# Kernel tuning notes

Hardware: AMD Instinct MI355X
Metric: run time of the kernel (lower is better)

Reference implementation:

```python
import jax, jax.numpy as jnp
import numpy as np

NEG_SLOPE = 0.2
EPS = 1e-16


def setup_inputs() -> dict:
    key = jax.random.key(0)
    k1, k2, k3, k4, k5 = jax.random.split(key, 5)
    N, E, F_IN, H, C = 100000, 1600000, 128, 4, 32
    x = jax.random.normal(k1, (N, F_IN), dtype=jnp.float32)
    edge_index = jax.random.randint(k2, (2, E), 0, N, dtype=jnp.int64)
    W = jax.random.normal(k3, (F_IN, H * C), dtype=jnp.float32) * (1.0 / np.sqrt(F_IN))
    att_src = jax.random.normal(k4, (H, C), dtype=jnp.float32) * 0.1
    att_dst = jax.random.normal(k5, (H, C), dtype=jnp.float32) * 0.1
    bias = jnp.zeros((H * C,), dtype=jnp.float32)
    return {"x": x, "edge_index": edge_index, "W": W, "att_src": att_src,
            "att_dst": att_dst, "bias": bias}


def reference(x, edge_index, W, att_src, att_dst, bias):
    N = x.shape[0]
    H, C = att_src.shape
    # PyG GATConv default: add self-loops
    loops = jnp.arange(N, dtype=edge_index.dtype)
    src = jnp.concatenate([edge_index[0], loops])  # [E+N]
    dst = jnp.concatenate([edge_index[1], loops])  # [E+N]

    h = (x @ W).reshape(N, H, C)                  # [N,H,C]
    a_src = jnp.einsum('nhc,hc->nh', h, att_src)  # [N,H]
    a_dst = jnp.einsum('nhc,hc->nh', h, att_dst)  # [N,H]

    e = a_src[src] + a_dst[dst]                   # [E',H]
    e = jax.nn.leaky_relu(e, NEG_SLOPE)

    # segment softmax over destination nodes (numerically stable)
    m = jax.ops.segment_max(e, dst, num_segments=N)      # [N,H]
    p = jnp.exp(e - m[dst])                               # [E',H]
    s = jax.ops.segment_sum(p, dst, num_segments=N)       # [N,H]
    alpha = p / (s[dst] + EPS)                             # [E',H]

    msg = h[src] * alpha[:, :, None]                       # [E',H,C]
    out = jax.ops.segment_sum(msg, dst, num_segments=N)   # [N,H,C]
    return out.reshape(N, H * C) + bias
```

## Files before the change

kernel.cpp:

```cpp
#include <hip/hip_runtime.h>
#include <stdint.h>


#define SLOT 64
#define CNTS 16
#define BCNS 16
#define BCAP 1536
#define MAXB 2048
#define KCH  8192

typedef __attribute__((ext_vector_type(8))) _Float16 h8;
typedef __attribute__((ext_vector_type(4))) float    f4x;

__device__ __forceinline__ float b2f(unsigned short u) {
    union { unsigned int i; float f; } v; v.i = ((unsigned int)u) << 16; return v.f;
}
__device__ __forceinline__ unsigned short f2b(float f) {
    union { float f; unsigned int i; } v; v.f = f;
    unsigned int i = v.i;
    unsigned int r = (i + 0x7FFFu + ((i >> 16) & 1u)) >> 16;
    return (unsigned short)r;
}
__device__ __forceinline__ unsigned short f2h(float f) {
    union { _Float16 h; unsigned short u; } v; v.h = (_Float16)f; return v.u;
}
__device__ __forceinline__ float h2f(unsigned short u) {
    union { _Float16 h; unsigned short u; } v; v.u = u; return (float)v.h;
}

__global__ void k_detect(const int* __restrict__ eidx, const unsigned int* __restrict__ xw,
                         int* flags) {
    __shared__ int nz, bf;
    if (threadIdx.x == 0) { nz = 0; bf = 0; }
    __syncthreads();
    int bad = 0;
    for (int i = threadIdx.x; i < 1024; i += 256)
        if (eidx[2 * i + 1] != 0) bad = 1;
    if (bad) atomicOr(&nz, 1);
    int hits = 0;
    for (int i = threadIdx.x; i < 4096; i += 256) {
        unsigned int e = (xw[i] >> 7) & 0xFFu;
        if (e >= 0x60u && e < 0xA0u) ++hits;
    }
    atomicAdd(&bf, hits);
    __syncthreads();
    if (threadIdx.x == 0) {
        flags[0] = (nz == 0) ? 1 : 0;
        flags[1] = (bf > 3072) ? 1 : 0;
    }
}

__device__ __forceinline__ int edge_at(const int* idx32, const long long* idx64,
                                       int is64, long long pos) {
    return is64 ? (int)idx64[pos] : idx32[pos];
}

__global__ void k_prep(const void* __restrict__ Wv, const void* __restrict__ asv,
                       const void* __restrict__ adv, const void* __restrict__ bv,
                       const int* __restrict__ flags,
                       _Float16* __restrict__ Wth, _Float16* __restrict__ Wtl,
                       float* __restrict__ attf , float* __restrict__ biasf ) {
    int isbf = flags[1];
    int tid = blockIdx.x * 256 + threadIdx.x;
    for (int i = tid; i < 16384; i += gridDim.x * 256) {
        int col = i >> 7, k = i & 127;
        float w = isbf ? b2f(((const unsigned short*)Wv)[k * 128 + col])
                       : ((const float*)Wv)[k * 128 + col];
        unsigned short hi = f2h(w);
        unsigned short lo = f2h(w - h2f(hi));
        ((unsigned short*)Wth)[i] = hi;
        ((unsigned short*)Wtl)[i] = lo;
    }
    if (blockIdx.x == 0) {
        for (int i = threadIdx.x; i < 128; i += 256) {
            attf[i]       = isbf ? b2f(((const unsigned short*)asv)[i]) : ((const float*)asv)[i];
            attf[128 + i] = isbf ? b2f(((const unsigned short*)adv)[i]) : ((const float*)adv)[i];
            biasf[i]      = isbf ? b2f(((const unsigned short*)bv)[i]) : ((const float*)bv)[i];
        }
    }
}

__global__ __launch_bounds__(256) void k_gemm_scatter(
    const void* __restrict__ xv,
    const _Float16* __restrict__ Wth, const _Float16* __restrict__ Wtl,
    const float* __restrict__ attf, const int* __restrict__ flags,
    unsigned short* __restrict__ hbf, float* __restrict__ asf,
    float* __restrict__ adf, int N,
    const int* __restrict__ idx32, const long long* __restrict__ idx64,
    int* __restrict__ bcnt, unsigned* __restrict__ bdat,
    int* __restrict__ cnt, int* __restrict__ esrc,
    int E, int Gg, int SB) {
    __shared__ unsigned short xsh[64 * 128];
    __shared__ unsigned short xsl[64 * 128];
    int tid = threadIdx.x;
    int bid = blockIdx.x;

    if (bid < SB) {
        int is64 = flags[0];
        int NBK = (N + 63) >> 6;
        long long e0 = (long long)bid * KCH;
        long long e1 = e0 + KCH; if (e1 > E) e1 = E;
        if (e0 >= E) return;

        if (NBK <= MAXB) {
            int wid = tid >> 6;
            int* h0 = (int*)xsh; int* h1 = h0 + MAXB;
            int* h2 = (int*)xsl; int* h3 = h2 + MAXB;
            int* hw = (wid == 0) ? h0 : (wid == 1) ? h1 : (wid == 2) ? h2 : h3;
            for (int i = tid; i < NBK; i += 256) { h0[i] = 0; h1[i] = 0; h2[i] = 0; h3[i] = 0; }
            __syncthreads();
            for (long long e = e0 + tid; e < e1; e += 256) {
                int d = is64 ? (int)idx64[(long long)E + e] : idx32[E + e];
                atomicAdd(&hw[d >> 6], 1);
            }
            __syncthreads();
            for (int b = tid; b < NBK; b += 256) {
                int c0 = h0[b], c1 = h1[b], c2 = h2[b], c3 = h3[b];
                int t = c0 + c1 + c2 + c3;
                int base = (t > 0) ? atomicAdd(&bcnt[(size_t)b * BCNS], t) : 0;
                h0[b] = base;
                h1[b] = base + c0;
                h2[b] = base + c0 + c1;
                h3[b] = base + c0 + c1 + c2;
            }
            __syncthreads();
            for (long long e = e0 + tid; e < e1; e += 256) {
                int d, s;
                if (is64) {
                    d = (int)idx64[(long long)E + e]; s = (int)idx64[e];
                } else {
                    d = idx32[E + e]; s = idx32[e];
                }
                int b = d >> 6;
                int p = atomicAdd(&hw[b], 1);
                if (p < BCAP)
                    bdat[(size_t)b * BCAP + p] = (unsigned)s | ((unsigned)(d & 63) << 26);
            }
        } else {
            for (long long e = e0 + tid; e < e1; e += 256) {
                int d = edge_at(idx32, idx64, is64, (long long)E + e);
                int s = edge_at(idx32, idx64, is64, e);
                int p = atomicAdd(&cnt[(size_t)d * CNTS], 1);
                if (p < SLOT) esrc[(size_t)d * SLOT + p] = s;
            }
        }
        return;
    }

    int rb = bid - SB;
    if (rb >= Gg) return;
    int r0 = rb * 64;
    int isbf = flags[1];
    int w = tid >> 6;
    int lane = tid & 63;
    int li = lane & 15;
    int g  = lane >> 4;
    int c0 = w * 32;

    h8 Bh[2][4], Bl[2][4];
#pragma unroll
    for (int t = 0; t < 2; ++t)
#pragma unroll
        for (int s = 0; s < 4; ++s) {
            size_t o = (size_t)(c0 + 16 * t + li) * 128 + 32 * s + 8 * g;
            Bh[t][s] = *(const h8*)(Wth + o);
            Bl[t][s] = *(const h8*)(Wtl + o);
        }

#pragma unroll
    for (int it = 0; it < 4; ++it) {
        int idx = it * 2048 + tid * 8;
        int r = idx >> 7, k = idx & 127;
        int gr = r0 + r; if (gr >= N) gr = N - 1;
        float v[8];
        if (isbf) {
            uint4 raw = *(const uint4*)((const unsigned short*)xv + (size_t)gr * 128 + k);
            v[0] = b2f((unsigned short)(raw.x & 0xFFFFu)); v[1] = b2f((unsigned short)(raw.x >> 16));
            v[2] = b2f((unsigned short)(raw.y & 0xFFFFu)); v[3] = b2f((unsigned short)(raw.y >> 16));
            v[4] = b2f((unsigned short)(raw.z & 0xFFFFu)); v[5] = b2f((unsigned short)(raw.z >> 16));
            v[6] = b2f((unsigned short)(raw.w & 0xFFFFu)); v[7] = b2f((unsigned short)(raw.w >> 16));
        } else {
            const float* xf = (const float*)xv;
            float4 a = *(const float4*)(xf + (size_t)gr * 128 + k);
            float4 b = *(const float4*)(xf + (size_t)gr * 128 + k + 4);
            v[0] = a.x; v[1] = a.y; v[2] = a.z; v[3] = a.w;
            v[4] = b.x; v[5] = b.y; v[6] = b.z; v[7] = b.w;
        }
        uint4 PH, PL;
        unsigned int ph[4], pl[4];
#pragma unroll
        for (int jj = 0; jj < 4; ++jj) {
            unsigned short h0 = f2h(v[2 * jj]), h1 = f2h(v[2 * jj + 1]);
            unsigned short l0 = f2h(v[2 * jj] - h2f(h0));
            unsigned short l1 = f2h(v[2 * jj + 1] - h2f(h1));
            ph[jj] = (unsigned int)h0 | ((unsigned int)h1 << 16);
            pl[jj] = (unsigned int)l0 | ((unsigned int)l1 << 16);
        }
        PH.x = ph[0]; PH.y = ph[1]; PH.z = ph[2]; PH.w = ph[3];
        PL.x = pl[0]; PL.y = pl[1]; PL.z = pl[2]; PL.w = pl[3];
        int off = r * 256 + ((2 * k) ^ ((r & 7) << 4));
        *(uint4*)((char*)xsh + off) = PH;
        *(uint4*)((char*)xsl + off) = PL;
    }
    __syncthreads();

    f4x acc[4][2];
#pragma unroll
    for (int m = 0; m < 4; ++m)
#pragma unroll
        for (int t = 0; t < 2; ++t) acc[m][t] = (f4x){0.f, 0.f, 0.f, 0.f};

#pragma unroll
    for (int s = 0; s < 4; ++s) {
#pragma unroll
        for (int m = 0; m < 4; ++m) {
            int row = 16 * m + li;
            int kb = (32 * s + 8 * g) * 2;
            int off = row * 256 + (kb ^ ((row & 7) << 4));
            h8 ah = *(const h8*)((const char*)xsh + off);
            h8 al = *(const h8*)((const char*)xsl + off);
#pragma unroll
            for (int t = 0; t < 2; ++t) {
                acc[m][t] = __builtin_amdgcn_mfma_f32_16x16x32_f16(ah, Bh[t][s], acc[m][t], 0, 0, 0);
                acc[m][t] = __builtin_amdgcn_mfma_f32_16x16x32_f16(al, Bh[t][s], acc[m][t], 0, 0, 0);
                acc[m][t] = __builtin_amdgcn_mfma_f32_16x16x32_f16(ah, Bl[t][s], acc[m][t], 0, 0, 0);
            }
        }
    }

    float at_s0 = attf[c0 + li],       at_s1 = attf[c0 + 16 + li];
    float at_d0 = attf[128 + c0 + li], at_d1 = attf[128 + c0 + 16 + li];
#pragma unroll
    for (int m = 0; m < 4; ++m) {
        float s1v[4], s2v[4];
#pragma unroll
        for (int j = 0; j < 4; ++j) {
            s1v[j] = acc[m][0][j] * at_s0 + acc[m][1][j] * at_s1;
            s2v[j] = acc[m][0][j] * at_d0 + acc[m][1][j] * at_d1;
        }
#pragma unroll
        for (int j = 0; j < 4; ++j) {
#pragma unroll
            for (int msk = 1; msk < 16; msk <<= 1) {
                s1v[j] += __shfl_xor(s1v[j], msk);
                s2v[j] += __shfl_xor(s2v[j], msk);
            }
        }
        if (li == 0) {
#pragma unroll
            for (int j = 0; j < 4; ++j) {
                int gr = r0 + 16 * m + 4 * g + j;
                if (gr < N) {
                    asf[(size_t)gr * 4 + w] = s1v[j];
                    adf[(size_t)gr * 4 + w] = s2v[j];
                }
            }
        }
    }

    __syncthreads();
#pragma unroll
    for (int m = 0; m < 4; ++m)
#pragma unroll
        for (int t = 0; t < 2; ++t)
#pragma unroll
            for (int j = 0; j < 4; ++j)
                xsh[(16 * m + 4 * g + j) * 128 + c0 + 16 * t + li] = f2b(acc[m][t][j]);
    __syncthreads();
#pragma unroll
    for (int it = 0; it < 4; ++it) {
        int u = it * 2048 + tid * 8;
        int r = u >> 7, k = u & 127;
        int gr = r0 + r;
        if (gr < N)
            *(uint4*)(hbf + (size_t)gr * 128 + k) = *(const uint4*)(xsh + u);
    }
}

template <int NB>
__device__ __forceinline__ void agg_node(
    int n, int dl, int deg, int lane, int head,
    const int lslot[64][SLOT], float* psh,
    const unsigned short* __restrict__ hbf,
    const float* __restrict__ asf, const float* __restrict__ adf,
    float& a0o, float& a1o, float& invho) {
    int sl = (lane == 0) ? n : ((lane <= deg) ? lslot[dl][lane - 1] : n);
    float4 av, adv;
    asm volatile("global_load_dwordx4 %0, %1, off"
                 : "=v"(av) : "v"((const void*)(asf + (size_t)sl * 4)));
    asm volatile("global_load_dwordx4 %0, %1, off"
                 : "=v"(adv) : "v"((const void*)(adf + (size_t)n * 4)));
    unsigned vv[NB * 8];
#pragma unroll
    for (int it = 0; it < NB * 8; ++it) {
        int s = (it == 0) ? n : ((it <= deg) ? lslot[dl][it - 1] : n);
        asm volatile("global_load_dword %0, %1, off"
                     : "=v"(vv[it]) : "v"((const void*)(hbf + (size_t)s * 128 + 2 * lane)));
    }
    asm volatile("s_waitcnt vmcnt(%0)" :: "n"(NB * 8));
    __builtin_amdgcn_sched_barrier(0);

    float p0 = 0.f, p1 = 0.f, p2 = 0.f, p3 = 0.f;
    if (lane <= deg) {
        float e0 = av.x + adv.x; e0 = fmaxf(e0, 0.2f * e0); p0 = __expf(e0);
        float e1 = av.y + adv.y; e1 = fmaxf(e1, 0.2f * e1); p1 = __expf(e1);
        float e2 = av.z + adv.z; e2 = fmaxf(e2, 0.2f * e2); p2 = __expf(e2);
        float e3 = av.w + adv.w; e3 = fmaxf(e3, 0.2f * e3); p3 = __expf(e3);
    }
    psh[0 * 64 + lane] = p0; psh[1 * 64 + lane] = p1;
    psh[2 * 64 + lane] = p2; psh[3 * 64 + lane] = p3;
    __builtin_amdgcn_wave_barrier();
    asm volatile("s_waitcnt lgkmcnt(0)" ::: "memory");
    __builtin_amdgcn_wave_barrier();

    float ps0 = p0, ps1 = p1, ps2 = p2, ps3 = p3;
#pragma unroll
    for (int m = 1; m < 64; m <<= 1) {
        ps0 += __shfl_xor(ps0, m);
        ps1 += __shfl_xor(ps1, m);
        ps2 += __shfl_xor(ps2, m);
        ps3 += __shfl_xor(ps3, m);
    }
    float den = head == 0 ? ps0 : head == 1 ? ps1 : head == 2 ? ps2 : ps3;
    invho = 1.0f / (den + 1e-16f);

    float a0 = 0.f, a1 = 0.f;
#pragma unroll
    for (int bi = 0; bi < NB; ++bi) {
        asm volatile("s_waitcnt vmcnt(%0)" :: "n"(8 * (NB - 1 - bi)));
        __builtin_amdgcn_sched_barrier(0);
        float4 qa = *(const float4*)(psh + head * 64 + bi * 8);
        float4 qb = *(const float4*)(psh + head * 64 + bi * 8 + 4);
#pragma unroll
        for (int k2 = 0; k2 < 8; ++k2) {
            float q = k2 < 4 ? qa[k2] : qb[k2 - 4];
            unsigned v = vv[bi * 8 + k2];
            a0 += q * b2f((unsigned short)v);
            a1 += q * b2f((unsigned short)(v >> 16));
        }
    }
    a0o = a0; a1o = a1;
}

__global__ __launch_bounds__(256) void k_bagg(
    const unsigned* __restrict__ bdat, const int* __restrict__ bcnt,
    const unsigned short* __restrict__ hbf,
    const float* __restrict__ asf, const float* __restrict__ adf,
    const int* __restrict__ idx32, const long long* __restrict__ idx64,
    const float* __restrict__ biasf, const int* __restrict__ flags,
    void* __restrict__ outv, int N, int E) {
    __shared__ int   lcnt[64];
    __shared__ int   lslot[64][SLOT];
    __shared__ float p_all[4][SLOT * 4];
    int b = blockIdx.x, tid = threadIdx.x;
    int wid = tid >> 6, lane = tid & 63, head = lane >> 4;

    if (tid < 64) lcnt[tid] = 0;
    __syncthreads();
    int mm = bcnt[(size_t)b * BCNS];
    int ovf = (mm > BCAP);
    if (mm > BCAP) mm = BCAP;
    for (int i = tid; i < mm; i += 256) {
        unsigned e = bdat[(size_t)b * BCAP + i];
        int dl = (int)(e >> 26);
        int p = atomicAdd(&lcnt[dl], 1);
        if (p < SLOT) lslot[dl][p] = (int)(e & 0x03FFFFFFu);
    }
    __syncthreads();

    float b0 = biasf[2 * lane], b1 = biasf[2 * lane + 1];
    float* psh = p_all[wid];
    int isbf = flags[1];
    int is64 = flags[0];

    for (int u = 0; u < 16; ++u) {
        int dl = wid * 16 + u;
        int n = (b << 6) + dl;
        if (n >= N) break;
        int deg = lcnt[dl];
        bool fb = ovf || (deg > SLOT - 1);
        float a0 = 0.f, a1 = 0.f, invh = 0.f;

        if (!fb && deg <= 31) {
            int nb = (deg + 8) >> 3;
            switch (nb) {
                case 1: agg_node<1>(n, dl, deg, lane, head, lslot, psh, hbf, asf, adf, a0, a1, invh); break;
                case 2: agg_node<2>(n, dl, deg, lane, head, lslot, psh, hbf, asf, adf, a0, a1, invh); break;
                case 3: agg_node<3>(n, dl, deg, lane, head, lslot, psh, hbf, asf, adf, a0, a1, invh); break;
                default: agg_node<4>(n, dl, deg, lane, head, lslot, psh, hbf, asf, adf, a0, a1, invh); break;
            }
        } else if (!fb) {
            float4 adv = *(const float4*)(adf + (size_t)n * 4);
            int sl = (lane == 0) ? n : ((lane <= deg) ? lslot[dl][lane - 1] : n);
            float4 av = *(const float4*)(asf + (size_t)sl * 4);
            float p0 = 0.f, p1 = 0.f, p2 = 0.f, p3 = 0.f;
            if (lane <= deg) {
                float e0 = av.x + adv.x; e0 = fmaxf(e0, 0.2f * e0); p0 = __expf(e0);
                float e1 = av.y + adv.y; e1 = fmaxf(e1, 0.2f * e1); p1 = __expf(e1);
                float e2 = av.z + adv.z; e2 = fmaxf(e2, 0.2f * e2); p2 = __expf(e2);
                float e3 = av.w + adv.w; e3 = fmaxf(e3, 0.2f * e3); p3 = __expf(e3);
            }
            psh[0 * 64 + lane] = p0; psh[1 * 64 + lane] = p1;
            psh[2 * 64 + lane] = p2; psh[3 * 64 + lane] = p3;
            __builtin_amdgcn_wave_barrier();
            asm volatile("s_waitcnt lgkmcnt(0)" ::: "memory");
            __builtin_amdgcn_wave_barrier();
            float ps0 = p0, ps1 = p1, ps2 = p2, ps3 = p3;
#pragma unroll
            for (int m = 1; m < 64; m <<= 1) {
                ps0 += __shfl_xor(ps0, m);
                ps1 += __shfl_xor(ps1, m);
                ps2 += __shfl_xor(ps2, m);
                ps3 += __shfl_xor(ps3, m);
            }
            float den = head == 0 ? ps0 : head == 1 ? ps1 : head == 2 ? ps2 : ps3;
            invh = 1.0f / (den + 1e-16f);
            int nb = (deg + 8) >> 3;
            for (int bi = 0; bi < nb; ++bi) {
                unsigned vt[8];
#pragma unroll
                for (int k2 = 0; k2 < 8; ++k2) {
                    int it = bi * 8 + k2;
                    int s = (it == 0) ? n : ((it <= deg) ? lslot[dl][it - 1] : n);
                    vt[k2] = *(const unsigned int*)(hbf + (size_t)s * 128 + 2 * lane);
                }
                float4 qa = *(const float4*)(psh + head * 64 + bi * 8);
                float4 qb = *(const float4*)(psh + head * 64 + bi * 8 + 4);
#pragma unroll
                for (int k2 = 0; k2 < 8; ++k2) {
                    float q = k2 < 4 ? qa[k2] : qb[k2 - 4];
                    a0 += q * b2f((unsigned short)vt[k2]);
                    a1 += q * b2f((unsigned short)(vt[k2] >> 16));
                }
            }
        } else {
            float4 adv = *(const float4*)(adf + (size_t)n * 4);
            float adh = head == 0 ? adv.x : head == 1 ? adv.y : head == 2 ? adv.z : adv.w;
            float den = 0.f;
            {
                float ev = asf[(size_t)n * 4 + head] + adh; ev = fmaxf(ev, 0.2f * ev);
                float p = __expf(ev);
                unsigned int v = *(const unsigned int*)(hbf + (size_t)n * 128 + 2 * lane);
                den += p;
                a0 += p * b2f((unsigned short)v);
                a1 += p * b2f((unsigned short)(v >> 16));
            }
            for (int e = 0; e < E; ++e) {
                int d = edge_at(idx32, idx64, is64, (long long)E + e);
                if (d == n) {
                    int s = edge_at(idx32, idx64, is64, e);
                    float ev = asf[(size_t)s * 4 + head] + adh; ev = fmaxf(ev, 0.2f * ev);
                    float p = __expf(ev);
                    unsigned int v = *(const unsigned int*)(hbf + (size_t)s * 128 + 2 * lane);
                    den += p;
                    a0 += p * b2f((unsigned short)v);
                    a1 += p * b2f((unsigned short)(v >> 16));
                }
            }
            invh = 1.0f / (den + 1e-16f);
        }

        a0 = a0 * invh + b0;
        a1 = a1 * invh + b1;
        if (isbf) {
            unsigned int pk = (unsigned int)f2b(a0) | ((unsigned int)f2b(a1) << 16);
            ((unsigned int*)outv)[(size_t)n * 64 + lane] = pk;
        } else {
            float2 f2; f2.x = a0; f2.y = a1;
            *(float2*)((float*)outv + (size_t)n * 128 + 2 * lane) = f2;
        }
        __builtin_amdgcn_wave_barrier();
    }
}

__global__ __launch_bounds__(256) void k_aggregate(
    const unsigned short* __restrict__ hbf,
    const float* __restrict__ asf, const float* __restrict__ adf,
    const int* __restrict__ cnt, const int* __restrict__ esrc,
    const int* __restrict__ idx32, const long long* __restrict__ idx64,
    const float* __restrict__ biasf, const int* __restrict__ flags,
    void* __restrict__ outv, int N, int E) {
    __shared__ float p_sh_all[4][SLOT * 4];
    __shared__ int   s_sh_all[4][SLOT];
    int wid = threadIdx.x >> 6;
    int lane = threadIdx.x & 63;
    int n = blockIdx.x * 4 + wid;
    if (n >= N) n = N - 1;
    float* p_sh = p_sh_all[wid];
    int*   s_sh = s_sh_all[wid];
    int head = lane >> 4;

    int deg = cnt[(size_t)n * CNTS];
    float4 adv = *(const float4*)(adf + (size_t)n * 4);
    bool fb = (deg > SLOT - 1);

    float p0 = 0.f, p1 = 0.f, p2 = 0.f, p3 = 0.f;
    if (!fb && lane <= deg) {
        int s = (lane == 0) ? n : esrc[(size_t)n * SLOT + lane - 1];
        float4 av = *(const float4*)(asf + (size_t)s * 4);
        float e0 = av.x + adv.x; e0 = fmaxf(e0, 0.2f * e0); p0 = __expf(e0);
        float e1 = av.y + adv.y; e1 = fmaxf(e1, 0.2f * e1); p1 = __expf(e1);
        float e2 = av.z + adv.z; e2 = fmaxf(e2, 0.2f * e2); p2 = __expf(e2);
        float e3 = av.w + adv.w; e3 = fmaxf(e3, 0.2f * e3); p3 = __expf(e3);
        s_sh[lane] = s;
        p_sh[lane * 4 + 0] = p0; p_sh[lane * 4 + 1] = p1;
        p_sh[lane * 4 + 2] = p2; p_sh[lane * 4 + 3] = p3;
    }
    __syncthreads();

    float b0 = biasf[2 * lane], b1 = biasf[2 * lane + 1];
    float a0 = 0.f, a1 = 0.f, invh;

    if (!fb) {
        float ps0 = p0, ps1 = p1, ps2 = p2, ps3 = p3;
#pragma unroll
        for (int m = 1; m < 64; m <<= 1) {
            ps0 += __shfl_xor(ps0, m);
            ps1 += __shfl_xor(ps1, m);
            ps2 += __shfl_xor(ps2, m);
            ps3 += __shfl_xor(ps3, m);
        }
        float den = head == 0 ? ps0 : head == 1 ? ps1 : head == 2 ? ps2 : ps3;
        invh = 1.0f / (den + 1e-16f);

        int tot = deg + 1;
        int i = 0;
        for (; i + 3 < tot; i += 4) {
            int s0 = s_sh[i], s1 = s_sh[i + 1], s2 = s_sh[i + 2], s3 = s_sh[i + 3];
            float q0 = p_sh[i * 4 + head],       q1 = p_sh[(i + 1) * 4 + head];
            float q2 = p_sh[(i + 2) * 4 + head], q3 = p_sh[(i + 3) * 4 + head];
            unsigned int v0 = *(const unsigned int*)(hbf + (size_t)s0 * 128 + 2 * lane);
            unsigned int v1 = *(const unsigned int*)(hbf + (size_t)s1 * 128 + 2 * lane);
            unsigned int v2 = *(const unsigned int*)(hbf + (size_t)s2 * 128 + 2 * lane);
            unsigned int v3 = *(const unsigned int*)(hbf + (size_t)s3 * 128 + 2 * lane);
            a0 += q0 * b2f((unsigned short)v0) + q1 * b2f((unsigned short)v1)
                + q2 * b2f((unsigned short)v2) + q3 * b2f((unsigned short)v3);
            a1 += q0 * b2f((unsigned short)(v0 >> 16)) + q1 * b2f((unsigned short)(v1 >> 16))
                + q2 * b2f((unsigned short)(v2 >> 16)) + q3 * b2f((unsigned short)(v3 >> 16));
        }
        for (; i < tot; ++i) {
            int s0 = s_sh[i];
            float q0 = p_sh[i * 4 + head];
            unsigned int v0 = *(const unsigned int*)(hbf + (size_t)s0 * 128 + 2 * lane);
            a0 += q0 * b2f((unsigned short)v0);
            a1 += q0 * b2f((unsigned short)(v0 >> 16));
        }
    } else {
        int is64 = flags[0];
        float adh = head == 0 ? adv.x : head == 1 ? adv.y : head == 2 ? adv.z : adv.w;
        float den = 0.f;
        {
            float ev = asf[(size_t)n * 4 + head] + adh; ev = fmaxf(ev, 0.2f * ev);
            float p = __expf(ev);
            unsigned int v = *(const unsigned int*)(hbf + (size_t)n * 128 + 2 * lane);
            den += p;
            a0 += p * b2f((unsigned short)v);
            a1 += p * b2f((unsigned short)(v >> 16));
        }
        for (int e = 0; e < E; ++e) {
            int d = edge_at(idx32, idx64, is64, (long long)E + e);
            if (d == n) {
                int s = edge_at(idx32, idx64, is64, e);
                float ev = asf[(size_t)s * 4 + head] + adh; ev = fmaxf(ev, 0.2f * ev);
                float p = __expf(ev);
                unsigned int v = *(const unsigned int*)(hbf + (size_t)s * 128 + 2 * lane);
                den += p;
                a0 += p * b2f((unsigned short)v);
                a1 += p * b2f((unsigned short)(v >> 16));
            }
        }
        invh = 1.0f / (den + 1e-16f);
    }

    a0 = a0 * invh + b0;
    a1 = a1 * invh + b1;
    if (flags[1]) {
        unsigned int pk = (unsigned int)f2b(a0) | ((unsigned int)f2b(a1) << 16);
        ((unsigned int*)outv)[(size_t)n * 64 + lane] = pk;
    } else {
        float2 f2; f2.x = a0; f2.y = a1;
        *(float2*)((float*)outv + (size_t)n * 128 + 2 * lane) = f2;
    }
}

extern "C" void kernel_launch(void* const* d_in, const int* in_sizes, int n_in,
                              void* d_out, int out_size, void* d_ws, size_t ws_size,
                              hipStream_t stream) {
    const void*      xv    = d_in[0];
    const int*       idx32 = (const int*)d_in[1];
    const long long* idx64 = (const long long*)d_in[1];

    int N = in_sizes[0] / 128;
    int E = in_sizes[1] / 2;

    char* ws = (char*)d_ws;
    size_t o = 0;
    auto alloc = [&](size_t bytes) {
        size_t r = o; o += (bytes + 255) & ~(size_t)255; return r;
    };
    unsigned short* hbf = (unsigned short*)(ws + alloc((size_t)N * 128 * 2));
    _Float16* Wth = (_Float16*)(ws + alloc(16384 * 2));
    _Float16* Wtl = (_Float16*)(ws + alloc(16384 * 2));
    float* attf  = (float*)(ws + alloc(256 * 4));
    float* biasf = (float*)(ws + alloc(128 * 4));
    float* asf   = (float*)(ws + alloc((size_t)N * 4 * 4));
    float* adf   = (float*)(ws + alloc((size_t)N * 4 * 4));
    int* cnt     = (int*)(ws + alloc((size_t)N * CNTS * 4));
    int* flags   = (int*)(ws + alloc(256));
    int* esrc    = (int*)(ws + alloc((size_t)N * SLOT * 4));
    int NBK = (N + 63) >> 6;
    int* bcnt      = (int*)(ws + alloc((size_t)NBK * BCNS * 4));
    unsigned* bdat = (unsigned*)(ws + alloc((size_t)NBK * BCAP * 4));

    int Gg = (N + 63) / 64;
    int SB = (E + KCH - 1) / KCH;
    int NB = SB + Gg;

    k_detect<<<1, 256, 0, stream>>>(idx32, (const unsigned int*)xv, flags);
    k_prep<<<16, 256, 0, stream>>>(d_in[2], d_in[3], d_in[4], d_in[5], flags, Wth, Wtl, attf, biasf);
    if (NBK <= MAXB) {
        hipMemsetAsync(bcnt, 0, (size_t)NBK * BCNS * 4, stream);
        k_gemm_scatter<<<NB, 256, 0, stream>>>(xv, Wth, Wtl, attf, flags, hbf, asf, adf, N,
                                               idx32, idx64, bcnt, bdat, cnt, esrc, E, Gg, SB);
        k_bagg<<<NBK, 256, 0, stream>>>(bdat, bcnt, hbf, asf, adf, idx32, idx64,
                                        biasf, flags, d_out, N, E);
    } else {
        hipMemsetAsync(cnt, 0, (size_t)N * CNTS * 4, stream);
        k_gemm_scatter<<<NB, 256, 0, stream>>>(xv, Wth, Wtl, attf, flags, hbf, asf, adf, N,
                                               idx32, idx64, bcnt, bdat, cnt, esrc, E, Gg, SB);
        k_aggregate<<<(N + 3) / 4, 256, 0, stream>>>(hbf, asf, adf, cnt, esrc, idx32, idx64,
                                                     biasf, flags, d_out, N, E);
    }
}
```

Before: 273.6 us.

## Split wave into two half-waves gathering alternate neighbors with dwordx2 loads

The common low-degree aggregation path now splits each 64-lane wave into two 32-lane halves. Each half handles alternate neighbor rows, and each lane loads 4 bf16 features with a dwordx2 load instead of 2 with a single dword. The halves are then combined with a cross-lane shuffle and only the lower half writes the output. This halves the number of serial gather load instructions per node and the template depth (NB 1-2 instead of 1-4). In exchange it adds a reduction shuffle, per-element LDS reads of attention weights, and a padded LDS stride (68).

Measured after the change: 254.0 us. -7.2%, faster.

```diff
diff --git a/kernel.cpp b/kernel.cpp
--- a/kernel.cpp
+++ b/kernel.cpp
@@ -8,9 +8,11 @@
 #define BCAP 1536
 #define MAXB 2048
 #define KCH  8192
+#define PST  68
 
 typedef __attribute__((ext_vector_type(8))) _Float16 h8;
 typedef __attribute__((ext_vector_type(4))) float    f4x;
+typedef __attribute__((ext_vector_type(2))) unsigned u32x2;
 
 __device__ __forceinline__ float b2f(unsigned short u) {
     union { unsigned int i; float f; } v; v.i = ((unsigned int)u) << 16; return v.f;
@@ -278,24 +280,28 @@
 }
 
 template <int NB>
-__device__ __forceinline__ void agg_node(
-    int n, int dl, int deg, int lane, int head,
+__device__ __forceinline__ void agg_node2(
+    int n, int dl, int deg, int lane,
     const int lslot[64][SLOT], float* psh,
     const unsigned short* __restrict__ hbf,
     const float* __restrict__ asf, const float* __restrict__ adf,
-    float& a0o, float& a1o, float& invho) {
+    float a[4], float& invho) {
+    int half = lane >> 5;
+    int cl = lane & 31;
+    int hd = cl >> 3;
     int sl = (lane == 0) ? n : ((lane <= deg) ? lslot[dl][lane - 1] : n);
     float4 av, adv;
     asm volatile("global_load_dwordx4 %0, %1, off"
                  : "=v"(av) : "v"((const void*)(asf + (size_t)sl * 4)));
     asm volatile("global_load_dwordx4 %0, %1, off"
                  : "=v"(adv) : "v"((const void*)(adf + (size_t)n * 4)));
-    unsigned vv[NB * 8];
-#pragma unroll
-    for (int it = 0; it < NB * 8; ++it) {
+    u32x2 vv[NB * 8];
+#pragma unroll
+    for (int k = 0; k < NB * 8; ++k) {
+        int it = 2 * k + half;
         int s = (it == 0) ? n : ((it <= deg) ? lslot[dl][it - 1] : n);
-        asm volatile("global_load_dword %0, %1, off"
-                     : "=v"(vv[it]) : "v"((const void*)(hbf + (size_t)s * 128 + 2 * lane)));
+        asm volatile("global_load_dwordx2 %0, %1, off"
+                     : "=v"(vv[k]) : "v"((const void*)(hbf + (size_t)s * 128 + 4 * cl)));
     }
     asm volatile("s_waitcnt vmcnt(%0)" :: "n"(NB * 8));
     __builtin_amdgcn_sched_barrier(0);
@@ -307,8 +313,8 @@
         float e2 = av.z + adv.z; e2 = fmaxf(e2, 0.2f * e2); p2 = __expf(e2);
         float e3 = av.w + adv.w; e3 = fmaxf(e3, 0.2f * e3); p3 = __expf(e3);
     }
-    psh[0 * 64 + lane] = p0; psh[1 * 64 + lane] = p1;
-    psh[2 * 64 + lane] = p2; psh[3 * 64 + lane] = p3;
+    psh[0 * PST + lane] = p0; psh[1 * PST + lane] = p1;
+    psh[2 * PST + lane] = p2; psh[3 * PST + lane] = p3;
     __builtin_amdgcn_wave_barrier();
     asm volatile("s_waitcnt lgkmcnt(0)" ::: "memory");
     __builtin_amdgcn_wave_barrier();
@@ -321,25 +327,24 @@
         ps2 += __shfl_xor(ps2, m);
         ps3 += __shfl_xor(ps3, m);
     }
-    float den = head == 0 ? ps0 : head == 1 ? ps1 : head == 2 ? ps2 : ps3;
+    float den = hd == 0 ? ps0 : hd == 1 ? ps1 : hd == 2 ? ps2 : ps3;
     invho = 1.0f / (den + 1e-16f);
 
-    float a0 = 0.f, a1 = 0.f;
 #pragma unroll
     for (int bi = 0; bi < NB; ++bi) {
         asm volatile("s_waitcnt vmcnt(%0)" :: "n"(8 * (NB - 1 - bi)));
         __builtin_amdgcn_sched_barrier(0);
-        float4 qa = *(const float4*)(psh + head * 64 + bi * 8);
-        float4 qb = *(const float4*)(psh + head * 64 + bi * 8 + 4);
 #pragma unroll
         for (int k2 = 0; k2 < 8; ++k2) {
-            float q = k2 < 4 ? qa[k2] : qb[k2 - 4];
-            unsigned v = vv[bi * 8 + k2];
-            a0 += q * b2f((unsigned short)v);
-            a1 += q * b2f((unsigned short)(v >> 16));
-        }
-    }
-    a0o = a0; a1o = a1;
+            int it = 2 * (bi * 8 + k2) + half;
+            float q = psh[hd * PST + it];
+            u32x2 v = vv[bi * 8 + k2];
+            a[0] += q * b2f((unsigned short)v[0]);
+            a[1] += q * b2f((unsigned short)(v[0] >> 16));
+            a[2] += q * b2f((unsigned short)v[1]);
+            a[3] += q * b2f((unsigned short)(v[1] >> 16));
+        }
+    }
 }
 
 __global__ __launch_bounds__(256) void k_bagg(
@@ -351,7 +356,7 @@
     void* __restrict__ outv, int N, int E) {
     __shared__ int   lcnt[64];
     __shared__ int   lslot[64][SLOT];
-    __shared__ float p_all[4][SLOT * 4];
+    __shared__ float p_all[4][4 * PST];
     int b = blockIdx.x, tid = threadIdx.x;
     int wid = tid >> 6, lane = tid & 63, head = lane >> 4;
 
@@ -368,7 +373,9 @@
     }
     __syncthreads();
 
+    int cl = lane & 31;
     float b0 = biasf[2 * lane], b1 = biasf[2 * lane + 1];
+    float4 bq4 = *(const float4*)(biasf + 4 * cl);
     float* psh = p_all[wid];
     int isbf = flags[1];
     int is64 = flags[0];
@@ -379,17 +386,30 @@
         if (n >= N) break;
         int deg = lcnt[dl];
         bool fb = ovf || (deg > SLOT - 1);
-        float a0 = 0.f, a1 = 0.f, invh = 0.f;
 
         if (!fb && deg <= 31) {
-            int nb = (deg + 8) >> 3;
-            switch (nb) {
-                case 1: agg_node<1>(n, dl, deg, lane, head, lslot, psh, hbf, asf, adf, a0, a1, invh); break;
-                case 2: agg_node<2>(n, dl, deg, lane, head, lslot, psh, hbf, asf, adf, a0, a1, invh); break;
-                case 3: agg_node<3>(n, dl, deg, lane, head, lslot, psh, hbf, asf, adf, a0, a1, invh); break;
-                default: agg_node<4>(n, dl, deg, lane, head, lslot, psh, hbf, asf, adf, a0, a1, invh); break;
+            float a4[4] = {0.f, 0.f, 0.f, 0.f};
+            float invh = 0.f;
+            int nb = (deg + 16) >> 4;
+            if (nb == 1) agg_node2<1>(n, dl, deg, lane, lslot, psh, hbf, asf, adf, a4, invh);
+            else         agg_node2<2>(n, dl, deg, lane, lslot, psh, hbf, asf, adf, a4, invh);
+#pragma unroll
+            for (int c = 0; c < 4; ++c) a4[c] += __shfl_xor(a4[c], 32);
+            float o0 = a4[0] * invh + bq4.x, o1 = a4[1] * invh + bq4.y;
+            float o2 = a4[2] * invh + bq4.z, o3 = a4[3] * invh + bq4.w;
+            if (lane < 32) {
+                if (isbf) {
+                    u32x2 pk;
+                    pk[0] = (unsigned)f2b(o0) | ((unsigned)f2b(o1) << 16);
+                    pk[1] = (unsigned)f2b(o2) | ((unsigned)f2b(o3) << 16);
+                    *(u32x2*)((unsigned*)outv + (size_t)n * 64 + cl * 2) = pk;
+                } else {
+                    float4 f4v; f4v.x = o0; f4v.y = o1; f4v.z = o2; f4v.w = o3;
+                    *(float4*)((float*)outv + (size_t)n * 128 + cl * 4) = f4v;
+                }
             }
         } else if (!fb) {
+            float a0 = 0.f, a1 = 0.f;
             float4 adv = *(const float4*)(adf + (size_t)n * 4);
             int sl = (lane == 0) ? n : ((lane <= deg) ? lslot[dl][lane - 1] : n);
             float4 av = *(const float4*)(asf + (size_t)sl * 4);
@@ -400,8 +420,8 @@
                 float e2 = av.z + adv.z; e2 = fmaxf(e2, 0.2f * e2); p2 = __expf(e2);
                 float e3 = av.w + adv.w; e3 = fmaxf(e3, 0.2f * e3); p3 = __expf(e3);
             }
-            psh[0 * 64 + lane] = p0; psh[1 * 64 + lane] = p1;
-            psh[2 * 64 + lane] = p2; psh[3 * 64 + lane] = p3;
+            psh[0 * PST + lane] = p0; psh[1 * PST + lane] = p1;
+            psh[2 * PST + lane] = p2; psh[3 * PST + lane] = p3;
             __builtin_amdgcn_wave_barrier();
             asm volatile("s_waitcnt lgkmcnt(0)" ::: "memory");
             __builtin_amdgcn_wave_barrier();
@@ -414,7 +434,7 @@
                 ps3 += __shfl_xor(ps3, m);
             }
             float den = head == 0 ? ps0 : head == 1 ? ps1 : head == 2 ? ps2 : ps3;
-            invh = 1.0f / (den + 1e-16f);
+            float invh = 1.0f / (den + 1e-16f);
             int nb = (deg + 8) >> 3;
             for (int bi = 0; bi < nb; ++bi) {
                 unsigned vt[8];
@@ -424,16 +444,24 @@
                     int s = (it == 0) ? n : ((it <= deg) ? lslot[dl][it - 1] : n);
                     vt[k2] = *(const unsigned int*)(hbf + (size_t)s * 128 + 2 * lane);
                 }
-                float4 qa = *(const float4*)(psh + head * 64 + bi * 8);
-                float4 qb = *(const float4*)(psh + head * 64 + bi * 8 + 4);
 #pragma unroll
                 for (int k2 = 0; k2 < 8; ++k2) {
-                    float q = k2 < 4 ? qa[k2] : qb[k2 - 4];
+                    float q = psh[head * PST + bi * 8 + k2];
                     a0 += q * b2f((unsigned short)vt[k2]);
                     a1 += q * b2f((unsigned short)(vt[k2] >> 16));
                 }
             }
+            a0 = a0 * invh + b0;
+            a1 = a1 * invh + b1;
+            if (isbf) {
+                unsigned int pk = (unsigned int)f2b(a0) | ((unsigned int)f2b(a1) << 16);
+                ((unsigned int*)outv)[(size_t)n * 64 + lane] = pk;
+            } else {
+                float2 f2; f2.x = a0; f2.y = a1;
+                *(float2*)((float*)outv + (size_t)n * 128 + 2 * lane) = f2;
+            }
         } else {
+            float a0 = 0.f, a1 = 0.f;
             float4 adv = *(const float4*)(adf + (size_t)n * 4);
             float adh = head == 0 ? adv.x : head == 1 ? adv.y : head == 2 ? adv.z : adv.w;
             float den = 0.f;
@@ -457,17 +485,16 @@
                     a1 += p * b2f((unsigned short)(v >> 16));
                 }
             }
-            invh = 1.0f / (den + 1e-16f);
-        }
-
-        a0 = a0 * invh + b0;
-        a1 = a1 * invh + b1;
-        if (isbf) {
-            unsigned int pk = (unsigned int)f2b(a0) | ((unsigned int)f2b(a1) << 16);
-            ((unsigned int*)outv)[(size_t)n * 64 + lane] = pk;
-        } else {
-            float2 f2; f2.x = a0; f2.y = a1;
-            *(float2*)((float*)outv + (size_t)n * 128 + 2 * lane) = f2;
+            float invh = 1.0f / (den + 1e-16f);
+            a0 = a0 * invh + b0;
+            a1 = a1 * invh + b1;
+            if (isbf) {
+                unsigned int pk = (unsigned int)f2b(a0) | ((unsigned int)f2b(a1) << 16);
+                ((unsigned int*)outv)[(size_t)n * 64 + lane] = pk;
+            } else {
+                float2 f2; f2.x = a0; f2.y = a1;
+                *(float2*)((float*)outv + (size_t)n * 128 + 2 * lane) = f2;
+            }
         }
         __builtin_amdgcn_wave_barrier();
     }
```
